# Performance work log

Hardware: AMD Instinct MI355X
Metric: run time of the kernel (lower is better)

The kernel has to match this reference:

```python
import jax, jax.numpy as jnp
import numpy as np

B, S, DN, L = 2048, 8, 8, 50        # batch, n_sparse, n_dense, hist len
V, VF = 100000, 100000              # sparse vocab, feed vocab
ED, FD = 16, 512                    # sparse embed dim, feed embed dim
HID1, HID2 = 256, 128               # DNN hidden sizes
NE, NT, EO = 8, 4, 8                # experts, tasks, expert out dim
INPUT_DIM = ED * S + DN + FD + FD   # 1160


def setup_inputs() -> dict:
    key = jax.random.key(0)
    ks = jax.random.split(key, 20)
    sc = 0.02
    f32 = jnp.float32
    return {
        "sparse_ids": jax.random.randint(ks[0], (B, S), 0, V),
        "dense": jax.random.normal(ks[1], (B, DN), f32),
        "feedid": jax.random.randint(ks[2], (B,), 0, VF),
        "hist_feedid": jax.random.randint(ks[3], (B, L), 0, VF),
        "emb_tables": jax.random.normal(ks[4], (S, V, ED), f32) * sc,
        "feed_table": jax.random.normal(ks[5], (VF, FD), f32) * sc,
        "attn_w1": jax.random.normal(ks[6], (4 * FD, 128), f32) * sc,
        "attn_b1": jnp.zeros((128,), f32),
        "attn_w2": jax.random.normal(ks[7], (128, 1), f32) * sc,
        "attn_b2": jnp.zeros((1,), f32),
        "dnn_w1": jax.random.normal(ks[8], (INPUT_DIM, HID1), f32) * sc,
        "dnn_b1": jnp.zeros((HID1,), f32),
        "dnn_w2": jax.random.normal(ks[9], (HID1, HID2), f32) * sc,
        "dnn_b2": jnp.zeros((HID2,), f32),
        "expert_w": jax.random.normal(ks[10], (NE, HID2, EO), f32) * sc,
        "gate_w": jax.random.normal(ks[11], (NT, HID2, NE), f32) * sc,
        "out_w": jax.random.normal(ks[12], (NT, EO, 1), f32) * sc,
        "out_b": jnp.zeros((NT, 1), f32),
    }


def reference(sparse_ids, dense, feedid, hist_feedid,
              emb_tables, feed_table,
              attn_w1, attn_b1, attn_w2, attn_b2,
              dnn_w1, dnn_b1, dnn_w2, dnn_b2,
              expert_w, gate_w, out_w, out_b):
    # --- sparse embeddings: one table per feature -> [B, S, ED] -> flat ---
    embed = jax.vmap(lambda t, ids: t[ids], in_axes=(0, 1), out_axes=1)(
        emb_tables, sparse_ids)                       # [B, S, ED]
    sparse_flat = embed.reshape(embed.shape[0], -1)   # [B, S*ED]

    # --- feed / history embeddings ---
    feed = feed_table[feedid]                         # [B, FD]
    hist = feed_table[hist_feedid]                    # [B, L, FD]

    # --- DIN attention (query=feed, keys=hist) ---
    q = jnp.broadcast_to(feed[:, None, :], hist.shape)          # [B, L, FD]
    x = jnp.concatenate([q, hist, q - hist, q * hist], axis=-1)  # [B, L, 4FD]
    h = jax.nn.relu(x @ attn_w1 + attn_b1)                       # [B, L, 128]
    scores = (h @ attn_w2 + attn_b2)[..., 0]                     # [B, L]
    attn = jax.nn.softmax(scores, axis=1)
    user_interest = jnp.einsum('bl,bld->bd', attn, hist)         # [B, FD]

    # --- DNN (dropout off in eval) ---
    dnn_in = jnp.concatenate([sparse_flat, dense, feed, user_interest], axis=1)
    z = jax.nn.relu(dnn_in @ dnn_w1 + dnn_b1)
    dnn_out = jax.nn.relu(z @ dnn_w2 + dnn_b2)                   # [B, 128]

    # --- MMOE (eval: no expert dropout mask) ---
    expert_out = jnp.einsum('bi,eio->beo', dnn_out, expert_w)    # [B, NE, EO]
    gates = jax.nn.softmax(jnp.einsum('bi,tie->bte', dnn_out, gate_w), axis=-1)
    task_out = jnp.einsum('bte,beo->bto', gates, expert_out)     # [B, NT, EO]

    # --- per-task heads ---
    logits = jnp.einsum('bto,toh->bth', task_out, out_w) + out_b  # [B, NT, 1]
    return jax.nn.sigmoid(logits)
```

## Files before the change

### kernel.cpp

```cpp
#include <hip/hip_runtime.h>
#include <hip/hip_bf16.h>

typedef unsigned short u16;
typedef unsigned int u32;
typedef __attribute__((ext_vector_type(8))) short short8;
typedef __attribute__((ext_vector_type(8))) u16 ushort8;
typedef __attribute__((ext_vector_type(4))) float f32x4;

#define BB 2048
#define SS 8
#define DNUM 8
#define LL 50
#define EDIM 16
#define FDIM 512
#define HID1 256
#define HID2 128
#define VF 100000
#define KDNN 1216
#define ROWS (BB*LL)

__device__ inline u16 f2bf(float x) {
    return __builtin_bit_cast(u16, __float2bfloat16(x));
}
__device__ inline float bf2f(u16 b) {
    u32 u = ((u32)b) << 16;
    return __builtin_bit_cast(float, u);
}
__device__ inline void load16_lds(const void* g, void* l) {
    __builtin_amdgcn_global_load_lds(
        (const __attribute__((address_space(1))) u32*)g,
        (__attribute__((address_space(3))) u32*)l, 16, 0, 0);
}
__device__ inline float wave_sum(float v) {
    #pragma unroll
    for (int off = 32; off > 0; off >>= 1) v += __shfl_xor(v, off, 64);
    return v;
}
__device__ inline float wave_max(float v) {
    #pragma unroll
    for (int off = 32; off > 0; off >>= 1) v = fmaxf(v, __shfl_xor(v, off, 64));
    return v;
}
__device__ inline void cvt8(const float4& a, const float4& b, ushort8& o) {
    o[0]=f2bf(a.x); o[1]=f2bf(a.y); o[2]=f2bf(a.z); o[3]=f2bf(a.w);
    o[4]=f2bf(b.x); o[5]=f2bf(b.y); o[6]=f2bf(b.z); o[7]=f2bf(b.w);
}

__global__ __launch_bounds__(256) void zero_flags(u32* __restrict__ f) {
    int i = blockIdx.x * 256 + threadIdx.x;
    if (i < 25024) f[i] = 0;
}

__global__ __launch_bounds__(256) void mark_used(
    const int* __restrict__ hist, const int* __restrict__ feedid,
    unsigned char* __restrict__ flags)
{
    int i = blockIdx.x * 256 + threadIdx.x;
    if (i < ROWS) flags[hist[i]] = 1;
    if (i < BB) flags[feedid[i]] = 1;
}

#define CVT_BLKS 25000
#define PREP_BLKS 2112
__global__ __launch_bounds__(256) void prep_all(
    const float* __restrict__ ft, u16* __restrict__ hb,
    const unsigned char* __restrict__ flags,
    const float* __restrict__ w1, const float* __restrict__ dw1,
    const float* __restrict__ dw2,
    u16* __restrict__ WHP_T, u16* __restrict__ WQ_T,
    u16* __restrict__ W1D_T, u16* __restrict__ W2D_T,
    const int* __restrict__ sparse_ids, const float* __restrict__ dense,
    const int* __restrict__ feedid, const float* __restrict__ emb_tables,
    u16* __restrict__ dnn_in, u16* __restrict__ A_q)
{
    int blk = blockIdx.x, t = threadIdx.x;
    if (blk < CVT_BLKS) {
        int r = blk * 4 + (t >> 6);
        if (flags[r]) {
            const float* src = ft + (size_t)r * FDIM + (t & 63) * 8;
            float4 a = *(const float4*)src;
            float4 b = *(const float4*)(src + 4);
            ushort8 o; cvt8(a, b, o);
            *(ushort8*)(hb + (size_t)r * FDIM + (t & 63) * 8) = o;
        }
    } else if (blk < CVT_BLKS + PREP_BLKS) {
        int idx = (blk - CVT_BLKS) * 256 + t;
        if (idx < 131072) {
            int n = idx >> 10, k = idx & 1023;
            float v;
            if (k < 512) v = w1[(512 + k) * 128 + n] - w1[(1024 + k) * 128 + n];
            else         v = w1[(1024 + k) * 128 + n];
            WHP_T[n * 1024 + k] = f2bf(v);
        } else if (idx < 196608) {
            int i = idx - 131072;
            int n = i >> 9, k = i & 511;
            WQ_T[n * 512 + k] = f2bf(w1[k * 128 + n] + w1[(1024 + k) * 128 + n]);
        } else if (idx < 507904) {
            int i = idx - 196608;
            int n = i / KDNN, k = i - n * KDNN;
            W1D_T[i] = (k < 1160) ? f2bf(dw1[k * HID1 + n]) : (u16)0;
        } else if (idx < 540672) {
            int i = idx - 507904;
            int n = i >> 8, k = i & 255;
            W2D_T[i] = f2bf(dw2[k * HID2 + n]);
        }
    } else {
        int b = blk - (CVT_BLKS + PREP_BLKS);
        u16* drow = dnn_in + (size_t)b * KDNN;
        if (t < 128) {
            int s = t >> 4, e = t & 15;
            int id = sparse_ids[b * SS + s];
            float v = emb_tables[(size_t)s * 1600000 + (size_t)id * EDIM + e];
            drow[t] = f2bf(v);
        } else if (t < 136) {
            drow[t] = f2bf(dense[b * DNUM + (t - 128)]);
        } else if (t < 192) {
            drow[1160 + (t - 136)] = 0;
        }
        int fid = feedid[b];
        float2 f = *(const float2*)&ft[(size_t)fid * FDIM + t * 2];
        u16 u0 = f2bf(f.x), u1 = f2bf(f.y);
        drow[136 + t * 2] = u0;
        drow[136 + t * 2 + 1] = u1;
        A_q[(size_t)b * FDIM + t * 2] = u0;
        A_q[(size_t)b * FDIM + t * 2 + 1] = u1;
    }
}

template<int BM, bool RELU, bool OUT_BF16>
__global__ __launch_bounds__(256, 4) void gemm_bt(
    const u16* __restrict__ A, int lda,
    const u16* __restrict__ BT, int ldb,
    const float* __restrict__ bias,
    void* __restrict__ Cv, int M, int N, int K)
{
    constexpr int MI = BM / 32;
    __shared__ u16 As[BM * 64];
    __shared__ u16 Bs[128 * 64];
    int m0 = blockIdx.x * BM, n0 = blockIdx.y * 128;
    int tid = threadIdx.x, wave = tid >> 6, lane = tid & 63;
    int lrow = lane >> 3, lk = (lane & 7) * 8;
    f32x4 acc[MI][4];
    f32x4 zz = {0.f, 0.f, 0.f, 0.f};
    #pragma unroll
    for (int i = 0; i < MI; i++)
        #pragma unroll
        for (int j = 0; j < 4; j++) acc[i][j] = zz;
    int wm = (wave >> 1) * (BM / 2), wn = (wave & 1) * 64;

    for (int kt = 0; kt < K; kt += 64) {
        #pragma unroll
        for (int j = 0; j < MI; ++j) {
            int c = wave * MI + j;
            int row = c * 8 + lrow;
            load16_lds(A + (size_t)(m0 + row) * lda + kt + lk, &As[c * 512]);
        }
        #pragma unroll
        for (int j = 0; j < 4; ++j) {
            int c = wave * 4 + j;
            int row = c * 8 + lrow;
            load16_lds(BT + (size_t)(n0 + row) * ldb + kt + lk, &Bs[c * 512]);
        }
        __syncthreads();
        #pragma unroll
        for (int ks = 0; ks < 2; ++ks) {
            int kk = ks * 32 + (lane >> 4) * 8;
            short8 af[MI], bf[4];
            #pragma unroll
            for (int i = 0; i < MI; i++)
                af[i] = *(const short8*)&As[(wm + i * 16 + (lane & 15)) * 64 + kk];
            #pragma unroll
            for (int j = 0; j < 4; j++)
                bf[j] = *(const short8*)&Bs[(wn + j * 16 + (lane & 15)) * 64 + kk];
            #pragma unroll
            for (int i = 0; i < MI; i++)
                #pragma unroll
                for (int j = 0; j < 4; j++)
                    acc[i][j] = __builtin_amdgcn_mfma_f32_16x16x32_bf16(
                        af[i], bf[j], acc[i][j], 0, 0, 0);
        }
        __syncthreads();
    }
    #pragma unroll
    for (int i = 0; i < MI; i++) {
        #pragma unroll
        for (int j = 0; j < 4; j++) {
            #pragma unroll
            for (int r = 0; r < 4; r++) {
                int row = m0 + wm + i * 16 + (lane >> 4) * 4 + r;
                int col = n0 + wn + j * 16 + (lane & 15);
                float v = acc[i][j][r];
                if (bias) v += bias[col];
                if (RELU) v = fmaxf(v, 0.f);
                size_t off = (size_t)row * N + col;
                if (OUT_BF16) ((u16*)Cv)[off] = f2bf(v);
                else ((float*)Cv)[off] = v;
            }
        }
    }
}

#define MFMA_BF16 __builtin_amdgcn_mfma_f32_16x16x32_bf16

__global__ __launch_bounds__(256, 4) void din_gemm(
    const int* __restrict__ hist_ids, const int* __restrict__ feedid,
    const u16* __restrict__ HB, const u16* __restrict__ WHP_T,
    const float* __restrict__ qw, const float* __restrict__ b1,
    const float* __restrict__ w2v, float* __restrict__ scores)
{
    __shared__ u16 As[64 * 32];
    __shared__ u16 BsH[128 * 32];
    __shared__ u16 BsP[128 * 32];
    __shared__ float qbs[3 * 128];
    __shared__ float w2s[128];
    __shared__ float sred[64 * 2];

    int t = threadIdx.x, w = t >> 6, lane = t & 63;
    int m0 = blockIdx.x * 64, b0 = m0 / LL;
    int fr = lane & 15, kg8 = (lane >> 4) * 8;
    int wm = (w >> 1) * 32, wn = (w & 1) * 64;

    for (int idx = t; idx < 384; idx += 256) {
        int bi = idx >> 7, col = idx & 127;
        int bb = b0 + bi; if (bb > BB - 1) bb = BB - 1;
        qbs[idx] = qw[bb * 128 + col] + b1[col];
    }
    if (t < 128) w2s[t] = w2v[t];

    const u16* a_src = HB + (size_t)hist_ids[m0 + w * 16 + (lane >> 2)] * FDIM
                          + (lane & 3) * 8;
    const u16* b_src0 = WHP_T + (size_t)(w * 32 + (lane >> 2)) * 1024 + (lane & 3) * 8;
    const u16* b_src1 = b_src0 + 16 * 1024;
    const u16* qp0 = HB + (size_t)feedid[(m0 + wm + fr) / LL] * FDIM + kg8;
    const u16* qp1 = HB + (size_t)feedid[(m0 + wm + 16 + fr) / LL] * FDIM + kg8;

    f32x4 acc[2][4];
    f32x4 zz = {0.f, 0.f, 0.f, 0.f};
    #pragma unroll
    for (int i = 0; i < 2; i++)
        #pragma unroll
        for (int j = 0; j < 4; j++) acc[i][j] = zz;

    for (int kt = 0; kt < 16; ++kt) {
        int ko = kt * 32;
        load16_lds(a_src + ko,        &As[w * 512]);
        load16_lds(b_src0 + ko,       &BsH[(w * 2) * 512]);
        load16_lds(b_src1 + ko,       &BsH[(w * 2 + 1) * 512]);
        load16_lds(b_src0 + 512 + ko, &BsP[(w * 2) * 512]);
        load16_lds(b_src1 + 512 + ko, &BsP[(w * 2 + 1) * 512]);
        __syncthreads();

        ushort8 qv0 = *(const ushort8*)(qp0 + ko);
        ushort8 qv1 = *(const ushort8*)(qp1 + ko);
        short8 ah0 = *(const short8*)&As[(wm + fr) * 32 + kg8];
        short8 ah1 = *(const short8*)&As[(wm + 16 + fr) * 32 + kg8];
        short8 bh[4], bp[4];
        #pragma unroll
        for (int j = 0; j < 4; ++j) {
            int n = wn + j * 16 + fr;
            bh[j] = *(const short8*)&BsH[n * 32 + kg8];
            bp[j] = *(const short8*)&BsP[n * 32 + kg8];
        }
        #pragma unroll
        for (int j = 0; j < 4; ++j) {
            acc[0][j] = MFMA_BF16(ah0, bh[j], acc[0][j], 0, 0, 0);
            acc[1][j] = MFMA_BF16(ah1, bh[j], acc[1][j], 0, 0, 0);
        }
        ushort8 hv0 = __builtin_bit_cast(ushort8, ah0);
        ushort8 hv1 = __builtin_bit_cast(ushort8, ah1);
        ushort8 pv0, pv1;
        #pragma unroll
        for (int e = 0; e < 8; ++e) {
            pv0[e] = f2bf(bf2f(hv0[e]) * bf2f(qv0[e]));
            pv1[e] = f2bf(bf2f(hv1[e]) * bf2f(qv1[e]));
        }
        short8 ap0 = __builtin_bit_cast(short8, pv0);
        short8 ap1 = __builtin_bit_cast(short8, pv1);
        #pragma unroll
        for (int j = 0; j < 4; ++j) {
            acc[0][j] = MFMA_BF16(ap0, bp[j], acc[0][j], 0, 0, 0);
            acc[1][j] = MFMA_BF16(ap1, bp[j], acc[1][j], 0, 0, 0);
        }
        __syncthreads();
    }

    #pragma unroll
    for (int i = 0; i < 2; ++i) {
        #pragma unroll
        for (int r = 0; r < 4; ++r) {
            int rl = wm + i * 16 + (lane >> 4) * 4 + r;
            int bi = (m0 + rl) / LL - b0;
            float s = 0.f;
            #pragma unroll
            for (int j = 0; j < 4; ++j) {
                int col = wn + j * 16 + fr;
                float v = acc[i][j][r] + qbs[bi * 128 + col];
                s += fmaxf(v, 0.f) * w2s[col];
            }
            s += __shfl_xor(s, 1, 64);
            s += __shfl_xor(s, 2, 64);
            s += __shfl_xor(s, 4, 64);
            s += __shfl_xor(s, 8, 64);
            if (fr == 0) sred[rl * 2 + (w & 1)] = s;
        }
    }
    __syncthreads();
    if (t < 64) scores[m0 + t] = sred[t * 2] + sred[t * 2 + 1];
}

__global__ __launch_bounds__(256) void softmax_ui(
    const float* __restrict__ scores, const int* __restrict__ hist_ids,
    const u16* __restrict__ HB, u16* __restrict__ dnn_in)
{
    int b = blockIdx.x, t = threadIdx.x;
    int wave = t >> 6, lane = t & 63;
    __shared__ float sc[56];
    __shared__ int hid[56];
    if (t >= 64 && t < 64 + LL) hid[t - 64] = hist_ids[b * LL + (t - 64)];
    if (wave == 0) {
        float x = (lane < LL) ? scores[b * LL + lane] : -1e30f;
        float mx = wave_max(x);
        float e = (lane < LL) ? __expf(x - mx) : 0.f;
        float s = wave_sum(e);
        if (lane < LL) sc[lane] = e / s;
    }
    __syncthreads();
    int d = t * 2;
    float a0 = 0.f, a1 = 0.f;
    #pragma unroll 5
    for (int l = 0; l < LL; ++l) {
        u32 v = *(const u32*)(HB + (size_t)hid[l] * FDIM + d);
        float al = sc[l];
        a0 += al * bf2f((u16)(v & 0xffff));
        a1 += al * bf2f((u16)(v >> 16));
    }
    dnn_in[(size_t)b * KDNN + 648 + d] = f2bf(a0);
    dnn_in[(size_t)b * KDNN + 648 + d + 1] = f2bf(a1);
}

__global__ __launch_bounds__(256) void mmoe_head(
    const float* __restrict__ dnn_out, const float* __restrict__ expert_w,
    const float* __restrict__ gate_w, const float* __restrict__ out_w,
    const float* __restrict__ out_b, float* __restrict__ out)
{
    int wave = threadIdx.x >> 6, lane = threadIdx.x & 63;
    int b = blockIdx.x * 4 + wave;
    __shared__ float ds[4][128];
    __shared__ float eo[4][64];
    __shared__ float gt[4][32];
    ds[wave][lane] = dnn_out[b * 128 + lane];
    ds[wave][lane + 64] = dnn_out[b * 128 + 64 + lane];
    __syncthreads();
    int e = lane >> 3, o = lane & 7;
    float acc = 0.f;
    for (int k = 0; k < 128; ++k)
        acc += ds[wave][k] * expert_w[(e * 128 + k) * 8 + o];
    eo[wave][lane] = acc;
    if (lane < 32) {
        int tt = lane >> 3, ee = lane & 7;
        float g = 0.f;
        for (int k = 0; k < 128; ++k)
            g += ds[wave][k] * gate_w[(tt * 128 + k) * 8 + ee];
        float m = g;
        #pragma unroll
        for (int off = 4; off; off >>= 1) m = fmaxf(m, __shfl_xor(m, off, 8));
        float ex = __expf(g - m);
        float s = ex;
        #pragma unroll
        for (int off = 4; off; off >>= 1) s += __shfl_xor(s, off, 8);
        gt[wave][lane] = ex / s;
    }
    __syncthreads();
    if (lane < 32) {
        int tt = lane >> 3, o2 = lane & 7;
        float to = 0.f;
        #pragma unroll
        for (int ee = 0; ee < 8; ++ee)
            to += gt[wave][tt * 8 + ee] * eo[wave][ee * 8 + o2];
        float pl = to * out_w[tt * 8 + o2];
        #pragma unroll
        for (int off = 4; off; off >>= 1) pl += __shfl_xor(pl, off, 8);
        if (o2 == 0) {
            float logit = pl + out_b[tt];
            out[b * 4 + tt] = 1.f / (1.f + __expf(-logit));
        }
    }
}

extern "C" void kernel_launch(void* const* d_in, const int* in_sizes, int n_in,
                              void* d_out, int out_size, void* d_ws, size_t ws_size,
                              hipStream_t stream)
{
    const int*   sparse_ids = (const int*)d_in[0];
    const float* dense      = (const float*)d_in[1];
    const int*   feedid     = (const int*)d_in[2];
    const int*   hist_ids   = (const int*)d_in[3];
    const float* emb_tables = (const float*)d_in[4];
    const float* feed_table = (const float*)d_in[5];
    const float* attn_w1    = (const float*)d_in[6];
    const float* attn_b1    = (const float*)d_in[7];
    const float* attn_w2    = (const float*)d_in[8];
    const float* attn_b2    = (const float*)d_in[9];
    const float* dnn_w1     = (const float*)d_in[10];
    const float* dnn_b1     = (const float*)d_in[11];
    const float* dnn_w2     = (const float*)d_in[12];
    const float* dnn_b2     = (const float*)d_in[13];
    const float* expert_w   = (const float*)d_in[14];
    const float* gate_w     = (const float*)d_in[15];
    const float* out_w      = (const float*)d_in[16];
    const float* out_b      = (const float*)d_in[17];
    float* out = (float*)d_out;

    char* ws = (char*)d_ws;
    size_t off = 0;
    auto alloc = [&](size_t bytes) {
        char* p = ws + off;
        off += (bytes + 255) & ~(size_t)255;
        return p;
    };
    u16* WHP_T = (u16*)alloc(131072 * 2);
    u16* WQ_T  = (u16*)alloc(65536 * 2);
    u16* W1D_T = (u16*)alloc((size_t)HID1 * KDNN * 2);
    u16* W2D_T = (u16*)alloc((size_t)HID2 * HID1 * 2);
    u16* AQ    = (u16*)alloc((size_t)BB * FDIM * 2);
    float* QW  = (float*)alloc((size_t)BB * 128 * 4);
    u16* DNNIN = (u16*)alloc((size_t)BB * KDNN * 2);
    u16* Z     = (u16*)alloc((size_t)BB * HID1 * 2);
    float* DOUT= (float*)alloc((size_t)BB * HID2 * 4);
    float* SCORES = (float*)alloc((size_t)ROWS * 4);
    unsigned char* FLAGS = (unsigned char*)alloc(100096);
    u16* HB16  = (u16*)alloc((size_t)VF * FDIM * 2);

    zero_flags<<<98, 256, 0, stream>>>((u32*)FLAGS);
    mark_used<<<400, 256, 0, stream>>>(hist_ids, feedid, FLAGS);
    prep_all<<<CVT_BLKS + PREP_BLKS + BB, 256, 0, stream>>>(
        feed_table, HB16, FLAGS, attn_w1, dnn_w1, dnn_w2,
        WHP_T, WQ_T, W1D_T, W2D_T,
        sparse_ids, dense, feedid, emb_tables, DNNIN, AQ);
    gemm_bt<32, false, false><<<dim3(BB / 32, 1), 256, 0, stream>>>(
        AQ, 512, WQ_T, 512, nullptr, QW, BB, 128, 512);
    din_gemm<<<ROWS / 64, 256, 0, stream>>>(
        hist_ids, feedid, HB16, WHP_T, QW, attn_b1, attn_w2, SCORES);
    softmax_ui<<<BB, 256, 0, stream>>>(SCORES, hist_ids, HB16, DNNIN);
    gemm_bt<32, true, true><<<dim3(BB / 32, HID1 / 128), 256, 0, stream>>>(
        DNNIN, KDNN, W1D_T, KDNN, dnn_b1, Z, BB, HID1, KDNN);
    gemm_bt<32, true, false><<<dim3(BB / 32, 1), 256, 0, stream>>>(
        Z, HID1, W2D_T, HID1, dnn_b2, DOUT, BB, HID2, HID1);
    mmoe_head<<<BB / 4, 256, 0, stream>>>(DOUT, expert_w, gate_w, out_w,
                                          out_b, out);
}
```

Measured before the change: 157.6 us.

## Double-buffer LDS tiles in gemm_bt and din_gemm to overlap loads with MFMA

Both the generic bf16 GEMM and the DIN attention GEMM now keep two LDS buffers per operand. Each iteration prefetches the next K tile into the other buffer before running the MFMAs on the current one. This is meant to hide global-to-LDS load latency behind compute instead of stalling at a barrier before each tile. In exchange it doubles the LDS footprint and lowers the launch-bounds occupancy hint from 4 to 3 blocks per CU, which may reduce latency hiding across blocks.

Measured after the change: 165.2 us. 1.05x slower.

```diff
diff --git a/kernel.cpp b/kernel.cpp
--- a/kernel.cpp
+++ b/kernel.cpp
@@ -128,15 +128,15 @@
 }
 
 template<int BM, bool RELU, bool OUT_BF16>
-__global__ __launch_bounds__(256, 4) void gemm_bt(
+__global__ __launch_bounds__(256, 3) void gemm_bt(
     const u16* __restrict__ A, int lda,
     const u16* __restrict__ BT, int ldb,
     const float* __restrict__ bias,
     void* __restrict__ Cv, int M, int N, int K)
 {
     constexpr int MI = BM / 32;
-    __shared__ u16 As[BM * 64];
-    __shared__ u16 Bs[128 * 64];
+    __shared__ u16 As[2][BM * 64];
+    __shared__ u16 Bs[2][128 * 64];
     int m0 = blockIdx.x * BM, n0 = blockIdx.y * 128;
     int tid = threadIdx.x, wave = tid >> 6, lane = tid & 63;
     int lrow = lane >> 3, lk = (lane & 7) * 8;
@@ -148,30 +148,37 @@
         for (int j = 0; j < 4; j++) acc[i][j] = zz;
     int wm = (wave >> 1) * (BM / 2), wn = (wave & 1) * 64;
 
-    for (int kt = 0; kt < K; kt += 64) {
+    auto stage = [&](int kt, int buf) {
         #pragma unroll
         for (int j = 0; j < MI; ++j) {
             int c = wave * MI + j;
             int row = c * 8 + lrow;
-            load16_lds(A + (size_t)(m0 + row) * lda + kt + lk, &As[c * 512]);
+            load16_lds(A + (size_t)(m0 + row) * lda + kt + lk, &As[buf][c * 512]);
         }
         #pragma unroll
         for (int j = 0; j < 4; ++j) {
             int c = wave * 4 + j;
             int row = c * 8 + lrow;
-            load16_lds(BT + (size_t)(n0 + row) * ldb + kt + lk, &Bs[c * 512]);
-        }
-        __syncthreads();
+            load16_lds(BT + (size_t)(n0 + row) * ldb + kt + lk, &Bs[buf][c * 512]);
+        }
+    };
+
+    stage(0, 0);
+    __syncthreads();
+    int nsteps = K / 64;
+    for (int s_ = 0; s_ < nsteps; ++s_) {
+        int buf = s_ & 1;
+        if (s_ + 1 < nsteps) stage((s_ + 1) * 64, buf ^ 1);
         #pragma unroll
         for (int ks = 0; ks < 2; ++ks) {
             int kk = ks * 32 + (lane >> 4) * 8;
             short8 af[MI], bf[4];
             #pragma unroll
             for (int i = 0; i < MI; i++)
-                af[i] = *(const short8*)&As[(wm + i * 16 + (lane & 15)) * 64 + kk];
+                af[i] = *(const short8*)&As[buf][(wm + i * 16 + (lane & 15)) * 64 + kk];
             #pragma unroll
             for (int j = 0; j < 4; j++)
-                bf[j] = *(const short8*)&Bs[(wn + j * 16 + (lane & 15)) * 64 + kk];
+                bf[j] = *(const short8*)&Bs[buf][(wn + j * 16 + (lane & 15)) * 64 + kk];
             #pragma unroll
             for (int i = 0; i < MI; i++)
                 #pragma unroll
@@ -202,15 +209,15 @@
 
 #define MFMA_BF16 __builtin_amdgcn_mfma_f32_16x16x32_bf16
 
-__global__ __launch_bounds__(256, 4) void din_gemm(
+__global__ __launch_bounds__(256, 3) void din_gemm(
     const int* __restrict__ hist_ids, const int* __restrict__ feedid,
     const u16* __restrict__ HB, const u16* __restrict__ WHP_T,
     const float* __restrict__ qw, const float* __restrict__ b1,
     const float* __restrict__ w2v, float* __restrict__ scores)
 {
-    __shared__ u16 As[64 * 32];
-    __shared__ u16 BsH[128 * 32];
-    __shared__ u16 BsP[128 * 32];
+    __shared__ u16 As[2][64 * 32];
+    __shared__ u16 BsH[2][128 * 32];
+    __shared__ u16 BsP[2][128 * 32];
     __shared__ float qbs[3 * 128];
     __shared__ float w2s[128];
     __shared__ float sred[64 * 2];
@@ -241,25 +248,33 @@
         #pragma unroll
         for (int j = 0; j < 4; j++) acc[i][j] = zz;
 
+    auto stage = [&](int ks, int buf) {
+        int ko = ks * 32;
+        load16_lds(a_src + ko,        &As[buf][w * 512]);
+        load16_lds(b_src0 + ko,       &BsH[buf][(w * 2) * 512]);
+        load16_lds(b_src1 + ko,       &BsH[buf][(w * 2 + 1) * 512]);
+        load16_lds(b_src0 + 512 + ko, &BsP[buf][(w * 2) * 512]);
+        load16_lds(b_src1 + 512 + ko, &BsP[buf][(w * 2 + 1) * 512]);
+    };
+
+    stage(0, 0);
+    __syncthreads();
+    #pragma unroll 2
     for (int kt = 0; kt < 16; ++kt) {
+        int buf = kt & 1;
         int ko = kt * 32;
-        load16_lds(a_src + ko,        &As[w * 512]);
-        load16_lds(b_src0 + ko,       &BsH[(w * 2) * 512]);
-        load16_lds(b_src1 + ko,       &BsH[(w * 2 + 1) * 512]);
-        load16_lds(b_src0 + 512 + ko, &BsP[(w * 2) * 512]);
-        load16_lds(b_src1 + 512 + ko, &BsP[(w * 2 + 1) * 512]);
-        __syncthreads();
+        if (kt < 15) stage(kt + 1, buf ^ 1);
 
         ushort8 qv0 = *(const ushort8*)(qp0 + ko);
         ushort8 qv1 = *(const ushort8*)(qp1 + ko);
-        short8 ah0 = *(const short8*)&As[(wm + fr) * 32 + kg8];
-        short8 ah1 = *(const short8*)&As[(wm + 16 + fr) * 32 + kg8];
+        short8 ah0 = *(const short8*)&As[buf][(wm + fr) * 32 + kg8];
+        short8 ah1 = *(const short8*)&As[buf][(wm + 16 + fr) * 32 + kg8];
         short8 bh[4], bp[4];
         #pragma unroll
         for (int j = 0; j < 4; ++j) {
             int n = wn + j * 16 + fr;
-            bh[j] = *(const short8*)&BsH[n * 32 + kg8];
-            bp[j] = *(const short8*)&BsP[n * 32 + kg8];
+            bh[j] = *(const short8*)&BsH[buf][n * 32 + kg8];
+            bp[j] = *(const short8*)&BsP[buf][n * 32 + kg8];
         }
         #pragma unroll
         for (int j = 0; j < 4; ++j) {
```

## Prefetch gathered A tiles one stage ahead and stage query rows in LDS

Applied to the files above, without the earlier changes.

The DIN attention GEMM now double-buffers the gathered history tile so the next A tile's global load is issued before the current iteration's weight loads complete. Manual waitcnt and barriers replace __syncthreads. The per-row query vectors are loaded once into shared memory instead of being re-read from global memory every k-iteration. The loop is fully unrolled. B tiles remain single-buffered, so the overlap only covers the random-gather A loads, and the hand-written vmcnt counts must match the load order exactly.

New measurement: 152.6 us. 1.03x faster.

```diff
diff --git a/kernel.cpp b/kernel.cpp
--- a/kernel.cpp
+++ b/kernel.cpp
@@ -208,9 +208,10 @@
     const float* __restrict__ qw, const float* __restrict__ b1,
     const float* __restrict__ w2v, float* __restrict__ scores)
 {
-    __shared__ u16 As[64 * 32];
+    __shared__ u16 As[2][64 * 32];
     __shared__ u16 BsH[128 * 32];
     __shared__ u16 BsP[128 * 32];
+    __shared__ u16 qls[3 * 512];
     __shared__ float qbs[3 * 128];
     __shared__ float w2s[128];
     __shared__ float sred[64 * 2];
@@ -231,8 +232,13 @@
                           + (lane & 3) * 8;
     const u16* b_src0 = WHP_T + (size_t)(w * 32 + (lane >> 2)) * 1024 + (lane & 3) * 8;
     const u16* b_src1 = b_src0 + 16 * 1024;
-    const u16* qp0 = HB + (size_t)feedid[(m0 + wm + fr) / LL] * FDIM + kg8;
-    const u16* qp1 = HB + (size_t)feedid[(m0 + wm + 16 + fr) / LL] * FDIM + kg8;
+
+    if (w < 3) {
+        int bb = b0 + w; if (bb > BB - 1) bb = BB - 1;
+        load16_lds(HB + (size_t)feedid[bb] * FDIM + lane * 8, &qls[w * 512]);
+    }
+    int qb0 = (m0 + wm + fr) / LL - b0;
+    int qb1 = (m0 + wm + 16 + fr) / LL - b0;
 
     f32x4 acc[2][4];
     f32x4 zz = {0.f, 0.f, 0.f, 0.f};
@@ -241,19 +247,23 @@
         #pragma unroll
         for (int j = 0; j < 4; j++) acc[i][j] = zz;
 
+    load16_lds(a_src,         &As[0][w * 512]);
+    load16_lds(b_src0,        &BsH[(w * 2) * 512]);
+    load16_lds(b_src1,        &BsH[(w * 2 + 1) * 512]);
+    load16_lds(b_src0 + 512,  &BsP[(w * 2) * 512]);
+    load16_lds(b_src1 + 512,  &BsP[(w * 2 + 1) * 512]);
+    load16_lds(a_src + 32,    &As[1][w * 512]);
+    asm volatile("s_waitcnt vmcnt(1) lgkmcnt(0)" ::: "memory");
+    __builtin_amdgcn_s_barrier();
+
+    #pragma unroll
     for (int kt = 0; kt < 16; ++kt) {
-        int ko = kt * 32;
-        load16_lds(a_src + ko,        &As[w * 512]);
-        load16_lds(b_src0 + ko,       &BsH[(w * 2) * 512]);
-        load16_lds(b_src1 + ko,       &BsH[(w * 2 + 1) * 512]);
-        load16_lds(b_src0 + 512 + ko, &BsP[(w * 2) * 512]);
-        load16_lds(b_src1 + 512 + ko, &BsP[(w * 2 + 1) * 512]);
-        __syncthreads();
-
-        ushort8 qv0 = *(const ushort8*)(qp0 + ko);
-        ushort8 qv1 = *(const ushort8*)(qp1 + ko);
-        short8 ah0 = *(const short8*)&As[(wm + fr) * 32 + kg8];
-        short8 ah1 = *(const short8*)&As[(wm + 16 + fr) * 32 + kg8];
+        const int buf = kt & 1;
+        const int ko = kt * 32;
+        short8 ah0 = *(const short8*)&As[buf][(wm + fr) * 32 + kg8];
+        short8 ah1 = *(const short8*)&As[buf][(wm + 16 + fr) * 32 + kg8];
+        ushort8 qv0 = *(const ushort8*)&qls[qb0 * 512 + ko + kg8];
+        ushort8 qv1 = *(const ushort8*)&qls[qb1 * 512 + ko + kg8];
         short8 bh[4], bp[4];
         #pragma unroll
         for (int j = 0; j < 4; ++j) {
@@ -281,7 +291,22 @@
             acc[0][j] = MFMA_BF16(ap0, bp[j], acc[0][j], 0, 0, 0);
             acc[1][j] = MFMA_BF16(ap1, bp[j], acc[1][j], 0, 0, 0);
         }
-        __syncthreads();
+        asm volatile("s_waitcnt lgkmcnt(0)" ::: "memory");
+        __builtin_amdgcn_s_barrier();
+        if (kt < 15) {
+            const int kn = (kt + 1) * 32;
+            load16_lds(b_src0 + kn,       &BsH[(w * 2) * 512]);
+            load16_lds(b_src1 + kn,       &BsH[(w * 2 + 1) * 512]);
+            load16_lds(b_src0 + 512 + kn, &BsP[(w * 2) * 512]);
+            load16_lds(b_src1 + 512 + kn, &BsP[(w * 2 + 1) * 512]);
+            if (kt < 14) {
+                load16_lds(a_src + (kt + 2) * 32, &As[buf][w * 512]);
+                asm volatile("s_waitcnt vmcnt(1)" ::: "memory");
+            } else {
+                asm volatile("s_waitcnt vmcnt(0)" ::: "memory");
+            }
+            __builtin_amdgcn_s_barrier();
+        }
     }
 
     #pragma unroll
```
